# Performance work log

Measured on AMD Instinct MI355X. Metric: run time of the kernel, lower is better.

Reference implementation:

```python
import jax, jax.numpy as jnp
import numpy as np

TEMPERATURE = 0.07
MARGIN = 0.15
HARD_NEG_RATIO = 0.5


def setup_inputs() -> dict:
    key = jax.random.key(0)
    k1, k2, k3 = jax.random.split(key, 3)
    B, D = 4096, 128
    drug_emb = jax.random.normal(k1, (B, D), dtype=jnp.float32)
    se_emb = jax.random.normal(k2, (B, D), dtype=jnp.float32)
    # labels spread over [0, 5) so that |diff| > 1.0 negatives exist
    labels = jax.random.uniform(k3, (B,), dtype=jnp.float32) * 5.0
    return {"drug_emb": drug_emb, "se_emb": se_emb, "labels": labels}


def _single_branch_loss(z, labels):
    B = z.shape[0]
    # F.normalize(z, dim=-1): divide by norm clamped to eps
    z = z / jnp.maximum(jnp.linalg.norm(z, axis=-1, keepdims=True), 1e-12)
    sim = jnp.matmul(z, z.T) / TEMPERATURE                      # [B, B]
    label_diff = jnp.abs(labels[None, :] - labels[:, None])     # [B, B]
    self_mask = ~jnp.eye(B, dtype=bool)
    pos_weight = jnp.exp(-label_diff / MARGIN) * self_mask      # soft positives
    neg_mask = (label_diff > 1.0) & self_mask

    # k = max(int(mean per-row negative count * ratio), 1), capped at B-1
    mean_negs = jnp.mean(jnp.sum(neg_mask.astype(jnp.float32), axis=1))
    k = jnp.maximum((mean_negs * HARD_NEG_RATIO).astype(jnp.int32), 1)
    k = jnp.minimum(k, B - 1)

    sim_max = jax.lax.stop_gradient(jnp.max(sim, axis=1, keepdims=True))
    logits = sim - sim_max

    # hard-negative top-k per row, as a static-shape rank test (jit-safe)
    neg_sim = jnp.where(neg_mask, sim, -jnp.inf)
    ranks = jnp.argsort(jnp.argsort(-neg_sim, axis=1), axis=1)  # 0 = largest
    hard_neg_mask = (ranks < k) & neg_mask

    any_neg = jnp.any(neg_mask)
    denom_mask = jnp.where(any_neg, hard_neg_mask | (pos_weight > 0.1), self_mask)

    exp_denom = jnp.sum(jnp.exp(logits) * denom_mask, axis=1, keepdims=True) + 1e-8
    log_prob = logits - jnp.log(exp_denom)
    weighted_log_prob = jnp.sum(pos_weight * log_prob, axis=1)
    denom = jnp.maximum(jnp.sum(pos_weight, axis=1), 1e-8)
    return -jnp.mean(weighted_log_prob / denom)


def reference(drug_emb, se_emb, labels):
    loss_drug = _single_branch_loss(drug_emb, labels)
    loss_se = _single_branch_loss(se_emb, labels)
    loss_cross = _single_branch_loss(drug_emb * se_emb, labels)
    return (loss_drug + loss_se + loss_cross) / 3.0
```

## Files before the change

kernel.cpp:

```cpp
#include <hip/hip_runtime.h>
#include <math.h>

#define BB 4096
#define DD 128
#define KLO 0x3E7FFFFFu
#define KHI 0xC1800000u
#define SH0 19
#define NBALLOC 4352

typedef __attribute__((ext_vector_type(8))) short bf16x8;
typedef __attribute__((ext_vector_type(4))) float f32x4;

__device__ __forceinline__ unsigned fkey(float x){
    int b = __float_as_int(x);
    return (unsigned)(b ^ ((b >> 31) | 0x80000000));
}
__device__ __forceinline__ float funkey(unsigned u){
    unsigned b = (u & 0x80000000u) ? (u & 0x7fffffffu) : ~u;
    return __uint_as_float(b);
}

__device__ __forceinline__ float blkSumF(float v, volatile float* sh){
    #pragma unroll
    for (int o = 32; o > 0; o >>= 1) v += __shfl_down(v, o);
    int t = threadIdx.x;
    __syncthreads();
    if ((t & 63) == 0) sh[t >> 6] = v;
    __syncthreads();
    return (sh[0] + sh[1]) + (sh[2] + sh[3]);
}
__device__ __forceinline__ int blkSumI(int v, volatile int* sh){
    #pragma unroll
    for (int o = 32; o > 0; o >>= 1) v += __shfl_down(v, o);
    int t = threadIdx.x;
    __syncthreads();
    if ((t & 63) == 0) sh[t >> 6] = v;
    __syncthreads();
    return (sh[0] + sh[1]) + (sh[2] + sh[3]);
}

__global__ void krn_normalize(const float* __restrict__ drug, const float* __restrict__ se,
                              const float* __restrict__ labels,
                              ushort* __restrict__ Z,
                              float* __restrict__ wp, float* __restrict__ wm){
    int row = blockIdx.x, br = blockIdx.y, t = threadIdx.x;
    float dv = drug[row * DD + t];
    float sv = se[row * DD + t];
    float v = (br == 0) ? dv : ((br == 1) ? sv : dv * sv);
    float sq = v * v;
    #pragma unroll
    for (int o = 32; o > 0; o >>= 1) sq += __shfl_down(sq, o);
    __shared__ float sh[2];
    if ((t & 63) == 0) sh[t >> 6] = sq;
    __syncthreads();
    float nrm = sqrtf(sh[0] + sh[1]);
    float outv = v / fmaxf(nrm, 1e-12f);
    unsigned u = __float_as_uint(outv);
    unsigned r = (u + 0x7FFFu + ((u >> 16) & 1u)) >> 16;
    int col = t ^ ((row & 7) << 3);
    Z[((size_t)br * BB + row) * DD + col] = (ushort)r;
    if (br == 0 && t == 0){
        float l = labels[row];
        wp[row] = __expf(l * (1.0f / 0.15f));
        wm[row] = __expf(l * (-1.0f / 0.15f));
    }
}

__global__ __launch_bounds__(256) void krn_labelstats(const float* __restrict__ labels,
                                                      int* __restrict__ NC,
                                                      float* __restrict__ PWS,
                                                      int* __restrict__ ntot){
    __shared__ float lab[BB];
    __shared__ int shi[4];
    __shared__ float shf[4];
    int t = threadIdx.x;
    #pragma unroll
    for (int e = 0; e < 4; ++e)
        ((float4*)lab)[t + e * 256] = ((const float4*)labels)[t + e * 256];
    __syncthreads();
    int i0 = blockIdx.x * 16;
    int ctot = 0;
    for (int ii = 0; ii < 16; ++ii){
        float li = lab[i0 + ii];
        int c = 0;
        float pws = 0.f;
        #pragma unroll
        for (int e = 0; e < 16; ++e){
            float d = fabsf(li - lab[t + e * 256]);
            c += (d > 1.0f) ? 1 : 0;
            pws += __expf(d * (-1.0f / 0.15f));
        }
        int C = blkSumI(c, shi);
        float P = blkSumF(pws, shf);
        if (t == 0){
            NC[i0 + ii] = C;
            PWS[i0 + ii] = P - 1.0f;
            ctot += C;
        }
    }
    if (t == 0) atomicAdd(ntot, ctot);
}

__global__ __launch_bounds__(256) void krn_masks(const float* __restrict__ labels,
                                                 ushort* __restrict__ negmask,
                                                 ushort* __restrict__ posmask){
    __shared__ float lab[BB];
    int t = threadIdx.x;
    #pragma unroll
    for (int e = 0; e < 4; ++e)
        ((float4*)lab)[t + e * 256] = ((const float4*)labels)[t + e * 256];
    __syncthreads();
    float lj[16];
    #pragma unroll
    for (int e = 0; e < 4; ++e)
        #pragma unroll
        for (int c = 0; c < 4; ++c)
            lj[e * 4 + c] = lab[4 * t + 1024 * e + c];
    int i0 = blockIdx.x * 16;
    for (int ii = 0; ii < 16; ++ii){
        int i = i0 + ii;
        float li = lab[i];
        unsigned nb = 0, pb = 0;
        #pragma unroll
        for (int e = 0; e < 4; ++e){
            #pragma unroll
            for (int c = 0; c < 4; ++c){
                int idx = e * 4 + c;
                int j = 4 * t + 1024 * e + c;
                float d = fabsf(li - lj[idx]);
                if (d > 1.0f) nb |= 1u << idx;
                else if (d < 0.34538776f && j != i) pb |= 1u << idx;
            }
        }
        negmask[i * 256 + t] = (ushort)nb;
        posmask[i * 256 + t] = (ushort)pb;
    }
}

__global__ void krn_calck(const int* __restrict__ ntot, int* __restrict__ kflags){
    int N = *ntot;
    int k = N >> 13;
    if (k < 1) k = 1;
    if (k > BB - 1) k = BB - 1;
    kflags[0] = k;
    kflags[1] = (N > 0) ? 1 : 0;
}

__device__ __forceinline__ bf16x8 frag_ld(const ushort* base, int row, int e0){
    int e = e0 ^ ((row & 7) << 3);
    return *(const bf16x8*)(base + row * DD + e);
}

__global__ __launch_bounds__(256) void krn_gemm(const ushort* __restrict__ Z,
                                                float* __restrict__ sim, size_t simStride,
                                                const float* __restrict__ wp,
                                                const float* __restrict__ wm,
                                                float* __restrict__ maxPart,
                                                float* __restrict__ psimPart,
                                                int r0){
    __shared__ ushort As[128 * DD];
    __shared__ ushort Bs[128 * DD];
    __shared__ float wpA[128], wmA[128], wpB[128], wmB[128];
    const ushort* Zb = Z + (size_t)blockIdx.z * (BB * DD);
    float* simz = sim + (size_t)blockIdx.z * simStride;
    int t = threadIdx.x;
    int rowbase = r0 + blockIdx.y * 128;
    int colbase = blockIdx.x * 128;

    {
        const float4* gA = (const float4*)(Zb + (size_t)rowbase * DD);
        const float4* gB = (const float4*)(Zb + (size_t)colbase * DD);
        float4* lA = (float4*)As;
        float4* lB = (float4*)Bs;
        #pragma unroll
        for (int it = 0; it < 8; ++it){
            lA[it * 256 + t] = gA[it * 256 + t];
            lB[it * 256 + t] = gB[it * 256 + t];
        }
        if (t < 128){
            wpA[t] = wp[rowbase + t];
            wmA[t] = wm[rowbase + t];
        } else {
            int u2 = t - 128;
            wpB[u2] = wp[colbase + u2];
            wmB[u2] = wm[colbase + u2];
        }
    }
    __syncthreads();

    int wid = t >> 6, lane = t & 63;
    int wr = (wid >> 1) * 64, wc = (wid & 1) * 64;
    int fr = lane & 15, fq = lane >> 4;

    f32x4 acc[4][4];
    #pragma unroll
    for (int m = 0; m < 4; ++m)
        #pragma unroll
        for (int n = 0; n < 4; ++n)
            acc[m][n] = (f32x4){0.f, 0.f, 0.f, 0.f};

    #pragma unroll
    for (int ks = 0; ks < 4; ++ks){
        int e0 = ks * 32 + fq * 8;
        bf16x8 a0 = frag_ld(As, wr + 0 * 16 + fr, e0);
        bf16x8 a1 = frag_ld(As, wr + 1 * 16 + fr, e0);
        bf16x8 a2 = frag_ld(As, wr + 2 * 16 + fr, e0);
        bf16x8 a3 = frag_ld(As, wr + 3 * 16 + fr, e0);
        bf16x8 b0 = frag_ld(Bs, wc + 0 * 16 + fr, e0);
        bf16x8 b1 = frag_ld(Bs, wc + 1 * 16 + fr, e0);
        bf16x8 b2 = frag_ld(Bs, wc + 2 * 16 + fr, e0);
        bf16x8 b3 = frag_ld(Bs, wc + 3 * 16 + fr, e0);
        acc[0][0] = __builtin_amdgcn_mfma_f32_16x16x32_bf16(a0, b0, acc[0][0], 0, 0, 0);
        acc[0][1] = __builtin_amdgcn_mfma_f32_16x16x32_bf16(a0, b1, acc[0][1], 0, 0, 0);
        acc[0][2] = __builtin_amdgcn_mfma_f32_16x16x32_bf16(a0, b2, acc[0][2], 0, 0, 0);
        acc[0][3] = __builtin_amdgcn_mfma_f32_16x16x32_bf16(a0, b3, acc[0][3], 0, 0, 0);
        acc[1][0] = __builtin_amdgcn_mfma_f32_16x16x32_bf16(a1, b0, acc[1][0], 0, 0, 0);
        acc[1][1] = __builtin_amdgcn_mfma_f32_16x16x32_bf16(a1, b1, acc[1][1], 0, 0, 0);
        acc[1][2] = __builtin_amdgcn_mfma_f32_16x16x32_bf16(a1, b2, acc[1][2], 0, 0, 0);
        acc[1][3] = __builtin_amdgcn_mfma_f32_16x16x32_bf16(a1, b3, acc[1][3], 0, 0, 0);
        acc[2][0] = __builtin_amdgcn_mfma_f32_16x16x32_bf16(a2, b0, acc[2][0], 0, 0, 0);
        acc[2][1] = __builtin_amdgcn_mfma_f32_16x16x32_bf16(a2, b1, acc[2][1], 0, 0, 0);
        acc[2][2] = __builtin_amdgcn_mfma_f32_16x16x32_bf16(a2, b2, acc[2][2], 0, 0, 0);
        acc[2][3] = __builtin_amdgcn_mfma_f32_16x16x32_bf16(a2, b3, acc[2][3], 0, 0, 0);
        acc[3][0] = __builtin_amdgcn_mfma_f32_16x16x32_bf16(a3, b0, acc[3][0], 0, 0, 0);
        acc[3][1] = __builtin_amdgcn_mfma_f32_16x16x32_bf16(a3, b1, acc[3][1], 0, 0, 0);
        acc[3][2] = __builtin_amdgcn_mfma_f32_16x16x32_bf16(a3, b2, acc[3][2], 0, 0, 0);
        acc[3][3] = __builtin_amdgcn_mfma_f32_16x16x32_bf16(a3, b3, acc[3][3], 0, 0, 0);
    }

    const float invT = 1.0f / 0.07f;
    int srow0 = blockIdx.y * 128 + wr + fq * 4;
    int scol0 = colbase + wc + fr;
    #pragma unroll
    for (int m = 0; m < 4; ++m){
        #pragma unroll
        for (int n = 0; n < 4; ++n){
            f32x4 c = acc[m][n];
            #pragma unroll
            for (int j = 0; j < 4; ++j)
                simz[(size_t)(srow0 + m * 16 + j) * BB + scol0 + n * 16] = c[j] * invT;
        }
    }

    float wpc[4], wmc[4];
    #pragma unroll
    for (int n = 0; n < 4; ++n){
        int cl = wc + n * 16 + fr;
        wpc[n] = wpB[cl];
        wmc[n] = wmB[cl];
    }
    size_t part = ((size_t)blockIdx.z * 64 + blockIdx.x * 2 + (wc ? 1 : 0)) * BB;
    float* maxP = maxPart + part;
    float* psiP = psimPart + part;
    #pragma unroll
    for (int m = 0; m < 4; ++m){
        #pragma unroll
        for (int j = 0; j < 4; ++j){
            int rl = wr + m * 16 + fq * 4 + j;
            float wpr = wpA[rl], wmr = wmA[rl];
            float mx = -INFINITY, ps = 0.f;
            #pragma unroll
            for (int n = 0; n < 4; ++n){
                float s = acc[m][n][j] * invT;
                mx = fmaxf(mx, s);
                float pw = fminf(wpr * wmc[n], wmr * wpc[n]);
                ps = fmaf(pw, s, ps);
            }
            #pragma unroll
            for (int o = 1; o < 16; o <<= 1){
                mx = fmaxf(mx, __shfl_xor(mx, o));
                ps += __shfl_xor(ps, o);
            }
            if (fr == 0){
                maxP[rowbase + rl] = mx;
                psiP[rowbase + rl] = ps;
            }
        }
    }
}

__global__ __launch_bounds__(256) void krn_reduceparts(const float* __restrict__ maxPart,
                                                       const float* __restrict__ psimPart,
                                                       float* __restrict__ Mrow,
                                                       float* __restrict__ PSIMrow,
                                                       int r0, int slab){
    int z = blockIdx.y;
    int lr = blockIdx.x * 256 + threadIdx.x;
    if (lr >= slab) return;
    int row = r0 + lr;
    float mx = -INFINITY, ps = 0.f;
    for (int bx = 0; bx < 64; ++bx){
        size_t off = ((size_t)z * 64 + bx) * BB + row;
        mx = fmaxf(mx, maxPart[off]);
        ps += psimPart[off];
    }
    Mrow[z * BB + row] = mx;
    PSIMrow[z * BB + row] = ps;
}

__global__ __launch_bounds__(256) void krn_stats(const float* __restrict__ sim, size_t simStride,
                                                 const ushort* __restrict__ negmask,
                                                 const ushort* __restrict__ posmask,
                                                 const float* __restrict__ Mrow,
                                                 const float* __restrict__ PSIMrow,
                                                 const float* __restrict__ PWSg,
                                                 const int* __restrict__ NCg,
                                                 const float* __restrict__ wp,
                                                 const float* __restrict__ wm,
                                                 const int* __restrict__ kflags,
                                                 float* __restrict__ rowloss, int r0){
    __shared__ int hist[NBALLOC];
    __shared__ int wsum[4];
    __shared__ float redf[4];
    __shared__ unsigned selb[3];
    __shared__ unsigned sel2[2];
    __shared__ int cnt;
    __shared__ unsigned list[96];

    int t = threadIdx.x;
    int bi = blockIdx.y;
    int row = blockIdx.x;
    int i = r0 + row;

    #pragma unroll
    for (int e = 0; e < 17; ++e) hist[t + e * 256] = 0;

    unsigned negU = negmask[i * 256 + t];
    unsigned posU = posmask[i * 256 + t];
    const float* srow = sim + (size_t)bi * simStride + (size_t)row * BB;
    const float4* sp = (const float4*)srow;

    float s[16];
    __syncthreads();

    #pragma unroll
    for (int e = 0; e < 4; ++e){
        float4 sv = sp[t + e * 256];
        s[e * 4 + 0] = sv.x; s[e * 4 + 1] = sv.y;
        s[e * 4 + 2] = sv.z; s[e * 4 + 3] = sv.w;
    }
    #pragma unroll
    for (int idx = 0; idx < 16; ++idx)
        if (negU & (1u << idx))
            atomicAdd(&hist[(fkey(s[idx]) - KLO) >> SH0], 1);
    __syncthreads();

    int kk = kflags[0], anyneg = kflags[1];
    int NCv = NCg[i];
    int mode = anyneg ? ((NCv <= kk) ? 1 : 0) : 2;

    unsigned ukth = 0;
    int rfin = 0;
    if (mode == 0){
        unsigned klo = KLO, khi = KHI;
        int sh = SH0;
        int rp = kk;
        bool ready = true;
        while (true){
            if (klo == khi){ ukth = klo; rfin = rp; break; }
            if (!ready){
                #pragma unroll
                for (int e = 0; e < 17; ++e) hist[t + e * 256] = 0;
                __syncthreads();
                #pragma unroll
                for (int idx = 0; idx < 16; ++idx){
                    if (negU & (1u << idx)){
                        unsigned u = fkey(s[idx]);
                        if (u >= klo && u <= khi)
                            atomicAdd(&hist[(u - klo) >> sh], 1);
                    }
                }
                __syncthreads();
            }
            ready = false;
            int g = 255 - t;
            int base = g * 17;
            int ls = 0;
            #pragma unroll
            for (int e = 0; e < 17; ++e) ls += hist[base + e];
            int v = ls;
            #pragma unroll
            for (int o = 1; o < 64; o <<= 1){
                int u2 = __shfl_up(v, o);
                if ((t & 63) >= o) v += u2;
            }
            if ((t & 63) == 63) wsum[t >> 6] = v;
            __syncthreads();
            int w = t >> 6;
            int pre = (w > 0 ? wsum[0] : 0) + (w > 1 ? wsum[1] : 0) + (w > 2 ? wsum[2] : 0);
            v += pre;
            int aec = v - ls;
            if (aec < rp && rp <= v){
                int cum = aec;
                #pragma unroll
                for (int e = 16; e >= 0; --e){
                    int c = hist[base + e];
                    if (cum < rp && rp <= cum + c){
                        selb[0] = (unsigned)(base + e);
                        selb[1] = (unsigned)cum;
                        selb[2] = (unsigned)c;
                        break;
                    }
                    cum += c;
                }
            }
            __syncthreads();
            unsigned B = selb[0];
            int ae = (int)selb[1];
            int c  = (int)selb[2];
            rp -= ae;
            klo += B << sh;
            unsigned nhi = klo + ((1u << sh) - 1u);
            if (nhi < khi) khi = nhi;
            if (c <= 96){
                if (t == 0) cnt = 0;
                __syncthreads();
                #pragma unroll
                for (int idx = 0; idx < 16; ++idx){
                    if (negU & (1u << idx)){
                        unsigned u = fkey(s[idx]);
                        if (u >= klo && u <= khi){
                            int p = atomicAdd(&cnt, 1);
                            list[p] = u;
                        }
                    }
                }
                __syncthreads();
                int cc = cnt;
                if (t < cc){
                    unsigned kj = list[t];
                    int g2 = 0, e2 = 0;
                    for (int mm = 0; mm < cc; ++mm){
                        unsigned km = list[mm];
                        g2 += (km > kj) ? 1 : 0;
                        e2 += (km == kj) ? 1 : 0;
                    }
                    if (g2 < rp && rp <= g2 + e2){ sel2[0] = kj; sel2[1] = (unsigned)g2; }
                }
                __syncthreads();
                ukth = sel2[0];
                rfin = rp - (int)sel2[1];
                break;
            }
            {
                unsigned range = khi - klo;
                int bits = 32 - __clz(range);
                sh = (bits > 12) ? (bits - 12) : 0;
            }
            __syncthreads();
        }
    }

    float M = Mrow[bi * BB + i];
    float skth = (mode == 0) ? funkey(ukth) : INFINITY;
    unsigned em = (mode == 2) ? 0xFFFFu : ((mode == 1) ? (negU | posU) : posU);
    float El = 0.f;
    #pragma unroll
    for (int idx = 0; idx < 16; ++idx){
        unsigned bit = 1u << idx;
        bool dm = (em & bit) != 0u;
        if (negU & bit) dm = dm || (s[idx] > skth);
        if (dm) El += __expf(s[idx] - M);
    }
    float Etot = blkSumF(El, redf);

    if (t == 0){
        if (mode == 0) Etot += (float)rfin * __expf(skth - M);
        float s_self = srow[i];
        if (mode == 2) Etot -= __expf(s_self - M);
        float PWSc  = PWSg[i];
        float PSIMc = PSIMrow[bi * BB + i] - (wp[i] * wm[i]) * s_self;
        float logE = __logf(Etot + 1e-8f);
        float wl = (PSIMc - M * PWSc) - PWSc * logE;
        rowloss[bi * BB + i] = wl / fmaxf(PWSc, 1e-8f);
    }
}

__global__ void krn_final(const float* __restrict__ rowloss, float* __restrict__ out){
    __shared__ float redf[4];
    int t = threadIdx.x;
    float total = 0.f;
    for (int b = 0; b < 3; ++b){
        float ssum = 0.f;
        for (int e = 0; e < 16; ++e) ssum += rowloss[b * BB + t + e * 256];
        float S = blkSumF(ssum, redf);
        total += S * (1.0f / BB);
    }
    if (t == 0) out[0] = -total / 3.0f;
}

extern "C" void kernel_launch(void* const* d_in, const int* in_sizes, int n_in,
                              void* d_out, int out_size, void* d_ws, size_t ws_size,
                              hipStream_t stream){
    const float* drug   = (const float*)d_in[0];
    const float* se     = (const float*)d_in[1];
    const float* labels = (const float*)d_in[2];
    float* out = (float*)d_out;
    char* ws = (char*)d_ws;

    const size_t zbytes = (size_t)3 * BB * DD * sizeof(ushort);
    const size_t tail = (size_t)(3 + 1 + 1 + 192 + 192 + 3 + 3 + 1 + 1) * BB * sizeof(float)
                      + (size_t)2 * BB * 256 * sizeof(ushort) + 256;

    int slab = BB;
    while (slab > 128 && zbytes + tail + (size_t)3 * slab * BB * sizeof(float) > ws_size)
        slab >>= 1;
    size_t simStride = (size_t)slab * BB;

    ushort* Z      = (ushort*)ws;
    float* simbuf  = (float*)(ws + zbytes);
    size_t off     = zbytes + (size_t)3 * simStride * sizeof(float);
    float* rowloss = (float*)(ws + off);  off += (size_t)3 * BB * sizeof(float);
    float* wp      = (float*)(ws + off);  off += (size_t)BB * sizeof(float);
    float* wm      = (float*)(ws + off);  off += (size_t)BB * sizeof(float);
    float* maxPart = (float*)(ws + off);  off += (size_t)192 * BB * sizeof(float);
    float* psimPart= (float*)(ws + off);  off += (size_t)192 * BB * sizeof(float);
    float* Mrow    = (float*)(ws + off);  off += (size_t)3 * BB * sizeof(float);
    float* PSIMrow = (float*)(ws + off);  off += (size_t)3 * BB * sizeof(float);
    float* PWSb    = (float*)(ws + off);  off += (size_t)BB * sizeof(float);
    int*   NCb     = (int*)(ws + off);    off += (size_t)BB * sizeof(int);
    ushort* negmask= (ushort*)(ws + off); off += (size_t)BB * 256 * sizeof(ushort);
    ushort* posmask= (ushort*)(ws + off); off += (size_t)BB * 256 * sizeof(ushort);
    int*   ntot    = (int*)(ws + off);
    int*   kflags  = ntot + 2;

    hipMemsetAsync(ntot, 0, 2 * sizeof(int), stream);
    krn_normalize<<<dim3(BB, 3), 128, 0, stream>>>(drug, se, labels, Z, wp, wm);
    krn_labelstats<<<256, 256, 0, stream>>>(labels, NCb, PWSb, ntot);
    krn_masks<<<256, 256, 0, stream>>>(labels, negmask, posmask);
    krn_calck<<<1, 1, 0, stream>>>(ntot, kflags);

    int nslab = BB / slab;
    for (int s2 = 0; s2 < nslab; ++s2){
        int r0 = s2 * slab;
        krn_gemm<<<dim3(BB / 128, slab / 128, 3), 256, 0, stream>>>(Z, simbuf, simStride,
                                                                    wp, wm, maxPart, psimPart, r0);
        krn_reduceparts<<<dim3((slab + 255) / 256, 3), 256, 0, stream>>>(maxPart, psimPart,
                                                                         Mrow, PSIMrow, r0, slab);
        krn_stats<<<dim3(slab, 3), 256, 0, stream>>>(simbuf, simStride, negmask, posmask,
                                                     Mrow, PSIMrow, PWSb, NCb, wp, wm,
                                                     kflags, rowloss, r0);
    }
    krn_final<<<1, 256, 0, stream>>>(rowloss, out);
}
```

Before: 195.8 us.

## Compute weighted positive-sim sums via sorted-label prefix sums, drop GEMM epilogue reductions

Labels are sorted by rank in the label-stats kernel. Because exp(-|li-lj|/margin) factorises as wp*wm products, each row's weighted similarity sum becomes a dot product of z_i with prefix and suffix sums of weighted embeddings over that sorted order. New prefix and psim kernels compute these sums, so the GEMM epilogue no longer does per-row max and weighted-sum partials, and the reduce-parts kernel is removed. The row max is taken as the diagonal self-similarity, which relies on unit-norm rows making the self term maximal. That holds up to bf16 rounding, and the prefix sums are accumulated in fp32 with exponential weights that can reach large magnitudes.

```diff
diff --git a/kernel.cpp b/kernel.cpp
--- a/kernel.cpp
+++ b/kernel.cpp
@@ -6,6 +6,7 @@
 #define KLO 0x3E7FFFFFu
 #define KHI 0xC1800000u
 #define SH0 19
+#define CHUNK 17
 #define NBALLOC 4352
 
 typedef __attribute__((ext_vector_type(8))) short bf16x8;
@@ -19,17 +20,11 @@
     unsigned b = (u & 0x80000000u) ? (u & 0x7fffffffu) : ~u;
     return __uint_as_float(b);
 }
+__device__ __forceinline__ float bf16f(ushort u){
+    return __uint_as_float(((unsigned)u) << 16);
+}
 
 __device__ __forceinline__ float blkSumF(float v, volatile float* sh){
-    #pragma unroll
-    for (int o = 32; o > 0; o >>= 1) v += __shfl_down(v, o);
-    int t = threadIdx.x;
-    __syncthreads();
-    if ((t & 63) == 0) sh[t >> 6] = v;
-    __syncthreads();
-    return (sh[0] + sh[1]) + (sh[2] + sh[3]);
-}
-__device__ __forceinline__ int blkSumI(int v, volatile int* sh){
     #pragma unroll
     for (int o = 32; o > 0; o >>= 1) v += __shfl_down(v, o);
     int t = threadIdx.x;
@@ -69,9 +64,10 @@
 __global__ __launch_bounds__(256) void krn_labelstats(const float* __restrict__ labels,
                                                       int* __restrict__ NC,
                                                       float* __restrict__ PWS,
+                                                      int* __restrict__ perm,
                                                       int* __restrict__ ntot){
     __shared__ float lab[BB];
-    __shared__ int shi[4];
+    __shared__ int shi[4], shr[4];
     __shared__ float shf[4];
     int t = threadIdx.x;
     #pragma unroll
@@ -81,20 +77,35 @@
     int i0 = blockIdx.x * 16;
     int ctot = 0;
     for (int ii = 0; ii < 16; ++ii){
-        float li = lab[i0 + ii];
-        int c = 0;
+        int i = i0 + ii;
+        float li = lab[i];
+        int c = 0, rk = 0;
         float pws = 0.f;
         #pragma unroll
         for (int e = 0; e < 16; ++e){
-            float d = fabsf(li - lab[t + e * 256]);
+            int j = t + e * 256;
+            float lj = lab[j];
+            float d = fabsf(li - lj);
             c += (d > 1.0f) ? 1 : 0;
             pws += __expf(d * (-1.0f / 0.15f));
-        }
-        int C = blkSumI(c, shi);
-        float P = blkSumF(pws, shf);
+            rk += (lj < li || (lj == li && j < i)) ? 1 : 0;
+        }
+        #pragma unroll
+        for (int o = 32; o > 0; o >>= 1){
+            c += __shfl_down(c, o);
+            rk += __shfl_down(rk, o);
+            pws += __shfl_down(pws, o);
+        }
+        __syncthreads();
+        if ((t & 63) == 0){ int w = t >> 6; shi[w] = c; shr[w] = rk; shf[w] = pws; }
+        __syncthreads();
         if (t == 0){
-            NC[i0 + ii] = C;
-            PWS[i0 + ii] = P - 1.0f;
+            int C = (shi[0] + shi[1]) + (shi[2] + shi[3]);
+            int R = (shr[0] + shr[1]) + (shr[2] + shr[3]);
+            float P = (shf[0] + shf[1]) + (shf[2] + shf[3]);
+            NC[i] = C;
+            PWS[i] = P - 1.0f;
+            perm[R] = i;
             ctot += C;
         }
     }
@@ -146,6 +157,99 @@
     kflags[1] = (N > 0) ? 1 : 0;
 }
 
+__global__ __launch_bounds__(256) void krn_prefix(const ushort* __restrict__ Z,
+                                                  const int* __restrict__ perm,
+                                                  const float* __restrict__ wp,
+                                                  const float* __restrict__ wm,
+                                                  float* __restrict__ Yt){
+    int d = blockIdx.x, b = blockIdx.y, t = threadIdx.x;
+    const ushort* Zb = Z + (size_t)b * BB * DD;
+    float uu[16], vv[16], wpj[16], wmj[16];
+    float tu = 0.f, tv = 0.f;
+    #pragma unroll
+    for (int q = 0; q < 16; ++q){
+        int r = t * 16 + q;
+        int j = perm[r];
+        int col = d ^ ((j & 7) << 3);
+        float zv = bf16f(Zb[j * DD + col]);
+        float a = wp[j], m2 = wm[j];
+        wpj[q] = a; wmj[q] = m2;
+        uu[q] = a * zv;  vv[q] = m2 * zv;
+        tu += uu[q];     tv += vv[q];
+    }
+    int lane = t & 63, w = t >> 6;
+    float xu = tu, xv = tv;
+    #pragma unroll
+    for (int o = 1; o < 64; o <<= 1){
+        float y1 = __shfl_up(xu, o);   if (lane >= o)      xu += y1;
+        float y2 = __shfl_down(xv, o); if (lane < 64 - o)  xv += y2;
+    }
+    __shared__ float wU[4], wV[4];
+    if (lane == 63) wU[w] = xu;
+    if (lane == 0)  wV[w] = xv;
+    __syncthreads();
+    float preU = 0.f, sufV = 0.f;
+    #pragma unroll
+    for (int ww = 0; ww < 4; ++ww){
+        if (ww < w) preU += wU[ww];
+        if (ww > w) sufV += wV[ww];
+    }
+    float offU   = preU + (xu - tu);
+    float exSufV = sufV + (xv - tv);
+    float acc = 0.f;
+    #pragma unroll
+    for (int q = 15; q >= 0; --q){
+        float S = exSufV + acc;
+        acc += vv[q];
+        vv[q] = S;
+    }
+    float* ytp = Yt + ((size_t)b * DD + d) * BB + t * 16;
+    acc = 0.f;
+    #pragma unroll
+    for (int q = 0; q < 16; ++q){
+        acc += uu[q];
+        float P = offU + acc;
+        ytp[q] = wmj[q] * P + wpj[q] * vv[q];
+    }
+}
+
+__global__ __launch_bounds__(256) void krn_psim(const ushort* __restrict__ Z,
+                                                const int* __restrict__ perm,
+                                                const float* __restrict__ wp,
+                                                const float* __restrict__ wm,
+                                                const float* __restrict__ Yt,
+                                                float* __restrict__ PSIMc){
+    int b = blockIdx.y, r0 = blockIdx.x * 32, t = threadIdx.x;
+    __shared__ float wt[32][129];
+    #pragma unroll
+    for (int q = 0; q < 16; ++q){
+        int idx = t * 16 + q;
+        int d = idx >> 5, r = idx & 31;
+        wt[r][d] = Yt[((size_t)b * DD + d) * BB + r0 + r];
+    }
+    __syncthreads();
+    int row = t >> 3, l8 = t & 7;
+    int j = perm[r0 + row];
+    const ushort* zr = Z + ((size_t)b * BB + j) * DD;
+    int swz = (j & 7) << 3;
+    float zy = 0.f, zz = 0.f;
+    #pragma unroll
+    for (int q = 0; q < 16; ++q){
+        int d = l8 * 16 + q;
+        float zv = bf16f(zr[d ^ swz]);
+        float wv = wt[row][d];
+        zy = fmaf(zv, wv, zy);
+        zz = fmaf(zv, zv, zz);
+    }
+    #pragma unroll
+    for (int o = 1; o < 8; o <<= 1){
+        zy += __shfl_xor(zy, o);
+        zz += __shfl_xor(zz, o);
+    }
+    if (l8 == 0)
+        PSIMc[(size_t)b * BB + j] = (zy - wp[j] * wm[j] * zz) * (1.0f / 0.07f);
+}
+
 __device__ __forceinline__ bf16x8 frag_ld(const ushort* base, int row, int e0){
     int e = e0 ^ ((row & 7) << 3);
     return *(const bf16x8*)(base + row * DD + e);
@@ -153,14 +257,9 @@
 
 __global__ __launch_bounds__(256) void krn_gemm(const ushort* __restrict__ Z,
                                                 float* __restrict__ sim, size_t simStride,
-                                                const float* __restrict__ wp,
-                                                const float* __restrict__ wm,
-                                                float* __restrict__ maxPart,
-                                                float* __restrict__ psimPart,
                                                 int r0){
     __shared__ ushort As[128 * DD];
     __shared__ ushort Bs[128 * DD];
-    __shared__ float wpA[128], wmA[128], wpB[128], wmB[128];
     const ushort* Zb = Z + (size_t)blockIdx.z * (BB * DD);
     float* simz = sim + (size_t)blockIdx.z * simStride;
     int t = threadIdx.x;
@@ -176,14 +275,6 @@
         for (int it = 0; it < 8; ++it){
             lA[it * 256 + t] = gA[it * 256 + t];
             lB[it * 256 + t] = gB[it * 256 + t];
-        }
-        if (t < 128){
-            wpA[t] = wp[rowbase + t];
-            wmA[t] = wm[rowbase + t];
-        } else {
-            int u2 = t - 128;
-            wpB[u2] = wp[colbase + u2];
-            wmB[u2] = wm[colbase + u2];
         }
     }
     __syncthreads();
@@ -241,72 +332,14 @@
                 simz[(size_t)(srow0 + m * 16 + j) * BB + scol0 + n * 16] = c[j] * invT;
         }
     }
-
-    float wpc[4], wmc[4];
-    #pragma unroll
-    for (int n = 0; n < 4; ++n){
-        int cl = wc + n * 16 + fr;
-        wpc[n] = wpB[cl];
-        wmc[n] = wmB[cl];
-    }
-    size_t part = ((size_t)blockIdx.z * 64 + blockIdx.x * 2 + (wc ? 1 : 0)) * BB;
-    float* maxP = maxPart + part;
-    float* psiP = psimPart + part;
-    #pragma unroll
-    for (int m = 0; m < 4; ++m){
-        #pragma unroll
-        for (int j = 0; j < 4; ++j){
-            int rl = wr + m * 16 + fq * 4 + j;
-            float wpr = wpA[rl], wmr = wmA[rl];
-            float mx = -INFINITY, ps = 0.f;
-            #pragma unroll
-            for (int n = 0; n < 4; ++n){
-                float s = acc[m][n][j] * invT;
-                mx = fmaxf(mx, s);
-                float pw = fminf(wpr * wmc[n], wmr * wpc[n]);
-                ps = fmaf(pw, s, ps);
-            }
-            #pragma unroll
-            for (int o = 1; o < 16; o <<= 1){
-                mx = fmaxf(mx, __shfl_xor(mx, o));
-                ps += __shfl_xor(ps, o);
-            }
-            if (fr == 0){
-                maxP[rowbase + rl] = mx;
-                psiP[rowbase + rl] = ps;
-            }
-        }
-    }
-}
-
-__global__ __launch_bounds__(256) void krn_reduceparts(const float* __restrict__ maxPart,
-                                                       const float* __restrict__ psimPart,
-                                                       float* __restrict__ Mrow,
-                                                       float* __restrict__ PSIMrow,
-                                                       int r0, int slab){
-    int z = blockIdx.y;
-    int lr = blockIdx.x * 256 + threadIdx.x;
-    if (lr >= slab) return;
-    int row = r0 + lr;
-    float mx = -INFINITY, ps = 0.f;
-    for (int bx = 0; bx < 64; ++bx){
-        size_t off = ((size_t)z * 64 + bx) * BB + row;
-        mx = fmaxf(mx, maxPart[off]);
-        ps += psimPart[off];
-    }
-    Mrow[z * BB + row] = mx;
-    PSIMrow[z * BB + row] = ps;
 }
 
 __global__ __launch_bounds__(256) void krn_stats(const float* __restrict__ sim, size_t simStride,
                                                  const ushort* __restrict__ negmask,
                                                  const ushort* __restrict__ posmask,
-                                                 const float* __restrict__ Mrow,
-                                                 const float* __restrict__ PSIMrow,
+                                                 const int* __restrict__ NCg,
                                                  const float* __restrict__ PWSg,
-                                                 const int* __restrict__ NCg,
-                                                 const float* __restrict__ wp,
-                                                 const float* __restrict__ wm,
+                                                 const float* __restrict__ PSIMg,
                                                  const int* __restrict__ kflags,
                                                  float* __restrict__ rowloss, int r0){
     __shared__ int hist[NBALLOC];
@@ -323,12 +356,17 @@
     int i = r0 + row;
 
     #pragma unroll
-    for (int e = 0; e < 17; ++e) hist[t + e * 256] = 0;
+    for (int e = 0; e < CHUNK; ++e) hist[t + e * 256] = 0;
 
     unsigned negU = negmask[i * 256 + t];
     unsigned posU = posmask[i * 256 + t];
     const float* srow = sim + (size_t)bi * simStride + (size_t)row * BB;
     const float4* sp = (const float4*)srow;
+    float M = srow[i];
+
+    int kk = kflags[0], anyneg = kflags[1];
+    int NCv = NCg[i];
+    int mode = anyneg ? ((NCv <= kk) ? 1 : 0) : 2;
 
     float s[16];
     __syncthreads();
@@ -343,11 +381,13 @@
     for (int idx = 0; idx < 16; ++idx)
         if (negU & (1u << idx))
             atomicAdd(&hist[(fkey(s[idx]) - KLO) >> SH0], 1);
-    __syncthreads();
-
-    int kk = kflags[0], anyneg = kflags[1];
-    int NCv = NCg[i];
-    int mode = anyneg ? ((NCv <= kk) ? 1 : 0) : 2;
+
+    unsigned em = (mode == 2) ? 0xFFFFu : ((mode == 1) ? (negU | posU) : posU);
+    float El = 0.f;
+    #pragma unroll
+    for (int idx = 0; idx < 16; ++idx)
+        if (em & (1u << idx)) El += __expf(s[idx] - M);
+    __syncthreads();
 
     unsigned ukth = 0;
     int rfin = 0;
@@ -360,7 +400,7 @@
             if (klo == khi){ ukth = klo; rfin = rp; break; }
             if (!ready){
                 #pragma unroll
-                for (int e = 0; e < 17; ++e) hist[t + e * 256] = 0;
+                for (int e = 0; e < CHUNK; ++e) hist[t + e * 256] = 0;
                 __syncthreads();
                 #pragma unroll
                 for (int idx = 0; idx < 16; ++idx){
@@ -374,10 +414,10 @@
             }
             ready = false;
             int g = 255 - t;
-            int base = g * 17;
+            int base = g * CHUNK;
             int ls = 0;
             #pragma unroll
-            for (int e = 0; e < 17; ++e) ls += hist[base + e];
+            for (int e = 0; e < CHUNK; ++e) ls += hist[base + e];
             int v = ls;
             #pragma unroll
             for (int o = 1; o < 64; o <<= 1){
@@ -393,7 +433,7 @@
             if (aec < rp && rp <= v){
                 int cum = aec;
                 #pragma unroll
-                for (int e = 16; e >= 0; --e){
+                for (int e = CHUNK - 1; e >= 0; --e){
                     int c = hist[base + e];
                     if (cum < rp && rp <= cum + c){
                         selb[0] = (unsigned)(base + e);
@@ -449,27 +489,20 @@
             }
             __syncthreads();
         }
-    }
-
-    float M = Mrow[bi * BB + i];
-    float skth = (mode == 0) ? funkey(ukth) : INFINITY;
-    unsigned em = (mode == 2) ? 0xFFFFu : ((mode == 1) ? (negU | posU) : posU);
-    float El = 0.f;
-    #pragma unroll
-    for (int idx = 0; idx < 16; ++idx){
-        unsigned bit = 1u << idx;
-        bool dm = (em & bit) != 0u;
-        if (negU & bit) dm = dm || (s[idx] > skth);
-        if (dm) El += __expf(s[idx] - M);
-    }
+        float skth = funkey(ukth);
+        #pragma unroll
+        for (int idx = 0; idx < 16; ++idx)
+            if ((negU & (1u << idx)) && s[idx] > skth)
+                El += __expf(s[idx] - M);
+    }
+
     float Etot = blkSumF(El, redf);
 
     if (t == 0){
-        if (mode == 0) Etot += (float)rfin * __expf(skth - M);
-        float s_self = srow[i];
-        if (mode == 2) Etot -= __expf(s_self - M);
+        if (mode == 0) Etot += (float)rfin * __expf(funkey(ukth) - M);
+        if (mode == 2) Etot -= 1.0f;
         float PWSc  = PWSg[i];
-        float PSIMc = PSIMrow[bi * BB + i] - (wp[i] * wm[i]) * s_self;
+        float PSIMc = PSIMg[(size_t)bi * BB + i];
         float logE = __logf(Etot + 1e-8f);
         float wl = (PSIMc - M * PWSc) - PWSc * logE;
         rowloss[bi * BB + i] = wl / fmaxf(PWSc, 1e-8f);
@@ -499,8 +532,10 @@
     char* ws = (char*)d_ws;
 
     const size_t zbytes = (size_t)3 * BB * DD * sizeof(ushort);
-    const size_t tail = (size_t)(3 + 1 + 1 + 192 + 192 + 3 + 3 + 1 + 1) * BB * sizeof(float)
-                      + (size_t)2 * BB * 256 * sizeof(ushort) + 256;
+    const size_t ytbytes = (size_t)3 * DD * BB * sizeof(float);
+    const size_t maskbytes = (size_t)BB * 256 * sizeof(ushort);
+    const size_t tail = (size_t)(3 + 3 + 1 + 1 + 1 + 1) * BB * sizeof(float)
+                      + ytbytes + 2 * maskbytes + 256;
 
     int slab = BB;
     while (slab > 128 && zbytes + tail + (size_t)3 * slab * BB * sizeof(float) > ws_size)
@@ -511,35 +546,31 @@
     float* simbuf  = (float*)(ws + zbytes);
     size_t off     = zbytes + (size_t)3 * simStride * sizeof(float);
     float* rowloss = (float*)(ws + off);  off += (size_t)3 * BB * sizeof(float);
+    float* PSIMc   = (float*)(ws + off);  off += (size_t)3 * BB * sizeof(float);
     float* wp      = (float*)(ws + off);  off += (size_t)BB * sizeof(float);
     float* wm      = (float*)(ws + off);  off += (size_t)BB * sizeof(float);
-    float* maxPart = (float*)(ws + off);  off += (size_t)192 * BB * sizeof(float);
-    float* psimPart= (float*)(ws + off);  off += (size_t)192 * BB * sizeof(float);
-    float* Mrow    = (float*)(ws + off);  off += (size_t)3 * BB * sizeof(float);
-    float* PSIMrow = (float*)(ws + off);  off += (size_t)3 * BB * sizeof(float);
     float* PWSb    = (float*)(ws + off);  off += (size_t)BB * sizeof(float);
     int*   NCb     = (int*)(ws + off);    off += (size_t)BB * sizeof(int);
-    ushort* negmask= (ushort*)(ws + off); off += (size_t)BB * 256 * sizeof(ushort);
-    ushort* posmask= (ushort*)(ws + off); off += (size_t)BB * 256 * sizeof(ushort);
+    int*   perm    = (int*)(ws + off);    off += (size_t)BB * sizeof(int);
+    float* Yt      = (float*)(ws + off);  off += ytbytes;
+    ushort* negmask= (ushort*)(ws + off); off += maskbytes;
+    ushort* posmask= (ushort*)(ws + off); off += maskbytes;
     int*   ntot    = (int*)(ws + off);
     int*   kflags  = ntot + 2;
 
     hipMemsetAsync(ntot, 0, 2 * sizeof(int), stream);
     krn_normalize<<<dim3(BB, 3), 128, 0, stream>>>(drug, se, labels, Z, wp, wm);
-    krn_labelstats<<<256, 256, 0, stream>>>(labels, NCb, PWSb, ntot);
+    krn_labelstats<<<256, 256, 0, stream>>>(labels, NCb, PWSb, perm, ntot);
     krn_masks<<<256, 256, 0, stream>>>(labels, negmask, posmask);
     krn_calck<<<1, 1, 0, stream>>>(ntot, kflags);
+    krn_prefix<<<dim3(DD, 3), 256, 0, stream>>>(Z, perm, wp, wm, Yt);
+    krn_psim<<<dim3(BB / 32, 3), 256, 0, stream>>>(Z, perm, wp, wm, Yt, PSIMc);
 
     int nslab = BB / slab;
     for (int s2 = 0; s2 < nslab; ++s2){
-        int r0 = s2 * slab;
-        krn_gemm<<<dim3(BB / 128, slab / 128, 3), 256, 0, stream>>>(Z, simbuf, simStride,
-                                                                    wp, wm, maxPart, psimPart, r0);
-        krn_reduceparts<<<dim3((slab + 255) / 256, 3), 256, 0, stream>>>(maxPart, psimPart,
-                                                                         Mrow, PSIMrow, r0, slab);
+        krn_gemm<<<dim3(BB / 128, slab / 128, 3), 256, 0, stream>>>(Z, simbuf, simStride, s2 * slab);
         krn_stats<<<dim3(slab, 3), 256, 0, stream>>>(simbuf, simStride, negmask, posmask,
-                                                     Mrow, PSIMrow, PWSb, NCb, wp, wm,
-                                                     kflags, rowloss, r0);
+                                                     NCb, PWSb, PSIMc, kflags, rowloss, s2 * slab);
     }
     krn_final<<<1, 256, 0, stream>>>(rowloss, out);
 }
```

Measured after the change: 189.4 us. 3.3% less time.
